# Performance work log

Hardware: AMD Instinct MI355X
Metric: run time of the kernel (lower is better)

The kernel has to match this reference:

```python
import jax, jax.numpy as jnp
import numpy as np

B, S, E, H, STEPS = 32, 2048, 300, 256, 24


def setup_inputs() -> dict:
    key = jax.random.key(0)
    ks = jax.random.split(key, 16)
    sc = 0.05
    inp = {
        "input_ids": jax.random.normal(ks[0], (B, S, E), dtype=jnp.float32),
        "tree_ids": jax.random.randint(ks[1], (B, STEPS, S), 0, S),
        "tree_ids_r": jax.random.randint(ks[2], (B, STEPS, S), 0, S),
        "tree_ids_l": jax.random.randint(ks[3], (B, STEPS, S), 0, S),
        # N-ary (binary) TreeLSTM parameters (Tai et al. 2015)
        "W_iou": jax.random.normal(ks[4], (E, 3 * H), dtype=jnp.float32) * sc,
        "b_iou": jnp.zeros((3 * H,), dtype=jnp.float32),
        "U_iou_l": jax.random.normal(ks[5], (H, 3 * H), dtype=jnp.float32) * sc,
        "U_iou_r": jax.random.normal(ks[6], (H, 3 * H), dtype=jnp.float32) * sc,
        "W_f": jax.random.normal(ks[7], (E, H), dtype=jnp.float32) * sc,
        "b_f": jnp.zeros((H,), dtype=jnp.float32),
        "U_f_ll": jax.random.normal(ks[8], (H, H), dtype=jnp.float32) * sc,
        "U_f_lr": jax.random.normal(ks[9], (H, H), dtype=jnp.float32) * sc,
        "U_f_rl": jax.random.normal(ks[10], (H, H), dtype=jnp.float32) * sc,
        "U_f_rr": jax.random.normal(ks[11], (H, H), dtype=jnp.float32) * sc,
    }
    return inp


def _gather_nodes(t, idx):
    # t: [B,S,H], idx: [B,S] -> [B,S,H]
    return jnp.take_along_axis(t, idx[..., None], axis=1)


def reference(input_ids, tree_ids, tree_ids_r, tree_ids_l,
              W_iou, b_iou, U_iou_l, U_iou_r,
              W_f, b_f, U_f_ll, U_f_lr, U_f_rl, U_f_rr):
    dt = input_ids.dtype
    h0 = jnp.zeros((B, S, H), dtype=dt)
    c0 = jnp.zeros((B, S, H), dtype=dt)
    # input projections are step-invariant: compute once
    x_iou = input_ids @ W_iou + b_iou          # [B,S,3H]
    x_f = input_ids @ W_f + b_f                # [B,S,H]
    bidx = jnp.arange(B)[:, None]              # [B,1]

    def step(carry, ids):
        h, c = carry
        idd, idl, idr = ids                    # each [B,S]
        h_l = _gather_nodes(h, idl); c_l = _gather_nodes(c, idl)
        h_r = _gather_nodes(h, idr); c_r = _gather_nodes(c, idr)
        iou = x_iou + h_l @ U_iou_l + h_r @ U_iou_r
        i, o, u = jnp.split(iou, 3, axis=-1)
        i = jax.nn.sigmoid(i); o = jax.nn.sigmoid(o); u = jnp.tanh(u)
        f_l = jax.nn.sigmoid(x_f + h_l @ U_f_ll + h_r @ U_f_lr)
        f_r = jax.nn.sigmoid(x_f + h_l @ U_f_rl + h_r @ U_f_rr)
        c_new = i * u + f_l * c_l + f_r * c_r
        h_new = o * jnp.tanh(c_new)
        # scatter updates to destination node ids; slot 0 is the null slot
        h = h.at[bidx, idd].set(h_new)
        c = c.at[bidx, idd].set(c_new)
        h = h.at[:, 0].set(0.0)
        c = c.at[:, 0].set(0.0)
        return (h, c), None

    ids_seq = (jnp.transpose(tree_ids, (1, 0, 2)),
               jnp.transpose(tree_ids_l, (1, 0, 2)),
               jnp.transpose(tree_ids_r, (1, 0, 2)))
    (h, c), _ = jax.lax.scan(step, (h0, c0), ids_seq)

    roots = tree_ids[:, -1, :].max(axis=1)     # [B]
    h_root = jnp.take_along_axis(
        h, jnp.broadcast_to(roots[:, None, None], (B, 1, H)), axis=1)[:, 0]
    return (h, c, h_root)
```

## Files before the change

### kernel.cpp

```cpp
#include <hip/hip_runtime.h>
#include <hip/hip_bf16.h>
#include <math.h>

#define B_     32
#define S_     2048
#define E_     300
#define H_     256
#define STEPS_ 24
#define BS_    (B_ * S_)
#define NPACK  1280
#define KSL    16
#define KSLP   10
#define COPYB  1024

typedef __bf16 bf16x8 __attribute__((ext_vector_type(8)));
typedef float  f32x4  __attribute__((ext_vector_type(4)));

__device__ __forceinline__ float sigm(float x) {
    return 1.0f / (1.0f + __expf(-x));
}
__device__ __forceinline__ float fast_tanh(float x) {
    return 2.0f * sigm(2.0f * x) - 1.0f;
}

__global__ __launch_bounds__(256) void pack_B_kernel(
    const float* __restrict__ U_iou_l, const float* __restrict__ U_iou_r,
    const float* __restrict__ U_f_ll,  const float* __restrict__ U_f_lr,
    const float* __restrict__ U_f_rl,  const float* __restrict__ U_f_rr,
    __hip_bfloat16* __restrict__ Bp)
{
    const int idx = blockIdx.x * 256 + threadIdx.x;
    if (idx >= KSL * NPACK * 32) return;
    const int ks = idx / (NPACK * 32);
    const int rem = idx - ks * (NPACK * 32);
    const int p = rem >> 5;
    const int kin = rem & 31;
    const int k = ks * 32 + kin;
    const int w = p / 80;
    const int rg = p - w * 80;
    const int g = rg >> 4;
    const int c = w * 16 + (rg & 15);
    float v;
    if (g < 3) {
        const int col = g * 256 + c;
        v = (k < 256) ? U_iou_l[k * 768 + col] : U_iou_r[(k - 256) * 768 + col];
    } else if (g == 3) {
        v = (k < 256) ? U_f_ll[k * 256 + c] : U_f_lr[(k - 256) * 256 + c];
    } else {
        v = (k < 256) ? U_f_rl[k * 256 + c] : U_f_rr[(k - 256) * 256 + c];
    }
    Bp[idx] = __float2bfloat16(v);
}

__global__ __launch_bounds__(256) void pack_W_kernel(
    const float* __restrict__ W_iou, const float* __restrict__ W_f,
    __hip_bfloat16* __restrict__ Wp)
{
    const int idx = blockIdx.x * 256 + threadIdx.x;
    if (idx >= KSLP * 1024 * 32) return;
    const int ks = idx / (1024 * 32);
    const int rem = idx - ks * (1024 * 32);
    const int p = rem >> 5;
    const int kin = rem & 31;
    const int k = ks * 32 + kin;
    const int cw = p >> 6;
    const int g = (p >> 4) & 3;
    const int col = cw * 16 + (p & 15);
    float v = 0.f;
    if (k < E_) v = (g < 3) ? W_iou[k * 768 + g * 256 + col] : W_f[k * 256 + col];
    Wp[idx] = __float2bfloat16(v);
}

__global__ __launch_bounds__(256) void winner_kernel(
    const int* __restrict__ tree_ids, int* __restrict__ winner)
{
    const int idx = blockIdx.x * 256 + threadIdx.x;
    if (idx >= B_ * STEPS_ * S_) return;
    const int b = idx / (STEPS_ * S_);
    const int rem = idx - b * (STEPS_ * S_);
    const int t = rem / S_;
    const int s = rem - t * S_;
    const int d = tree_ids[idx];
    if ((unsigned)d < (unsigned)S_)
        atomicMax(&winner[(size_t)t * BS_ + b * S_ + d], s);
}

__global__ __launch_bounds__(256) void compact_kernel(
    const int* __restrict__ winner, int* __restrict__ compact,
    int* __restrict__ count)
{
    const int tb = blockIdx.x;
    const int tid = threadIdx.x;
    const int* w = winner + (size_t)tb * S_;
    int* cmp = compact + (size_t)tb * S_;
    __shared__ int scan_[256];
    __shared__ int base_;
    if (tid == 0) base_ = 0;
    __syncthreads();
    for (int chunk = 0; chunk < S_ / 256; ++chunk) {
        const int d = chunk * 256 + tid;
        const int s = w[d];
        const int p = (d != 0 && s >= 0) ? 1 : 0;
        int v = p;
        scan_[tid] = v;
        __syncthreads();
        for (int off = 1; off < 256; off <<= 1) {
            const int add = (tid >= off) ? scan_[tid - off] : 0;
            __syncthreads();
            v += add;
            scan_[tid] = v;
            __syncthreads();
        }
        const int mybase = base_;
        if (p) cmp[mybase + v - 1] = (s << 11) | d;
        __syncthreads();
        if (tid == 0) base_ += scan_[255];
        __syncthreads();
    }
    if (tid == 0) count[tb] = base_;
}

__global__ __launch_bounds__(256) void proj_kernel(
    const float* __restrict__ input, const __hip_bfloat16* __restrict__ Wp,
    const float* __restrict__ b_iou, const float* __restrict__ b_f,
    __hip_bfloat16* __restrict__ x_pack)
{
    __shared__ __hip_bfloat16 Ash[16][328];
    const int tid = threadIdx.x;
    const int row0 = blockIdx.x * 16;

    for (int it = 0; it < 5; ++it) {
        const int idx = tid + it * 256;
        const int r = idx / 80;
        const int c4 = idx - r * 80;
        float4 v = make_float4(0.f, 0.f, 0.f, 0.f);
        if (c4 < 75) v = *(const float4*)(input + (size_t)(row0 + r) * E_ + c4 * 4);
        union { __hip_bfloat16 h[4]; uint2 u; } tconv;
        tconv.h[0] = __float2bfloat16(v.x);
        tconv.h[1] = __float2bfloat16(v.y);
        tconv.h[2] = __float2bfloat16(v.z);
        tconv.h[3] = __float2bfloat16(v.w);
        *(uint2*)&Ash[r][c4 * 4] = tconv.u;
    }
    __syncthreads();

    const int lane = tid & 63;
    const int wave = tid >> 6;
    const int m16 = lane & 15;
    const int q = lane >> 4;

    f32x4 acc[16];
    const f32x4 z4 = {0.f, 0.f, 0.f, 0.f};
#pragma unroll
    for (int nt = 0; nt < 16; ++nt) acc[nt] = z4;

    const __hip_bfloat16* wp = Wp + ((size_t)(wave * 256 + m16)) * 32 + q * 8;
    for (int ks = 0; ks < KSLP; ++ks) {
        const bf16x8 a = *reinterpret_cast<const bf16x8*>(&Ash[m16][ks * 32 + q * 8]);
        const __hip_bfloat16* wk = wp + (size_t)ks * 32768;
#pragma unroll
        for (int nt = 0; nt < 16; ++nt) {
            const bf16x8 bb = *reinterpret_cast<const bf16x8*>(wk + nt * 512);
            acc[nt] = __builtin_amdgcn_mfma_f32_16x16x32_bf16(a, bb, acc[nt], 0, 0, 0);
        }
    }

#pragma unroll
    for (int j = 0; j < 4; ++j) {
        const int row = row0 + q * 4 + j;
        const size_t xrow = (size_t)row * 1024;
#pragma unroll
        for (int chunk = 0; chunk < 4; ++chunk) {
            const int c = (wave * 4 + chunk) * 16 + m16;
            union { __hip_bfloat16 h[4]; uint2 u; } pk;
            pk.h[0] = __float2bfloat16(acc[chunk * 4 + 0][j] + b_iou[c]);
            pk.h[1] = __float2bfloat16(acc[chunk * 4 + 1][j] + b_iou[256 + c]);
            pk.h[2] = __float2bfloat16(acc[chunk * 4 + 2][j] + b_iou[512 + c]);
            pk.h[3] = __float2bfloat16(acc[chunk * 4 + 3][j] + b_f[c]);
            *(uint2*)(x_pack + xrow + (size_t)c * 4) = pk.u;
        }
    }
}

__global__ __launch_bounds__(256, 3) void step_kernel(
    const __hip_bfloat16* __restrict__ h_cur, const __hip_bfloat16* __restrict__ c_cur,
    __hip_bfloat16* __restrict__ h_next, __hip_bfloat16* __restrict__ c_next,
    const int* __restrict__ tree_ids_l, const int* __restrict__ tree_ids_r,
    const int* __restrict__ winner_t, const int* __restrict__ compact,
    const int* __restrict__ count, const __hip_bfloat16* __restrict__ x_pack,
    const __hip_bfloat16* __restrict__ Bp, int t)
{
    const int tid = threadIdx.x;

    if (blockIdx.x < COPYB) {
        const uint4* h_cur4 = (const uint4*)h_cur;
        const uint4* c_cur4 = (const uint4*)c_cur;
        uint4* h_next4 = (uint4*)h_next;
        uint4* c_next4 = (uint4*)c_next;
#pragma unroll
        for (int i = 0; i < 8; ++i) {
            const int idx = blockIdx.x * 256 + tid + i * (COPYB * 256);
            const int row = idx >> 5;
            const int d = row & (S_ - 1);
            if (d == 0) {
                const uint4 z = make_uint4(0u, 0u, 0u, 0u);
                h_next4[idx] = z;
                c_next4[idx] = z;
            } else if (winner_t[row] < 0) {
                h_next4[idx] = h_cur4[idx];
                c_next4[idx] = c_cur4[idx];
            }
        }
        return;
    }

    const int sb     = blockIdx.x - COPYB;
    const int grp    = sb >> 4;
    const int l16    = sb & 15;
    const int nh     = l16 >> 3;
    const int tile_g = grp * 8 + (l16 & 7);
    const int b    = tile_g >> 6;
    const int tile = tile_g & 63;
    const int nAct = count[t * B_ + b];
    const int s0 = tile * 32;
    if (s0 >= nAct) return;

    __shared__ __hip_bfloat16 Ash[32][520];
    __shared__ __hip_bfloat16 Csh[2][32][136];
    __shared__ int sS[32], sD[32], sIdl[32], sIdr[32];

    const int* cmp = compact + ((size_t)(t * B_ + b)) * S_;
    if (tid < 32) {
        const int gi = s0 + tid;
        const int pair = (gi < nAct) ? cmp[gi] : 0;
        sS[tid] = pair >> 11;
        sD[tid] = pair & 2047;
    }
    __syncthreads();

    const int* idl_b = tree_ids_l + ((size_t)b * STEPS_ + t) * S_;
    const int* idr_b = tree_ids_r + ((size_t)b * STEPS_ + t) * S_;
    if (tid < 32)       sIdl[tid]      = idl_b[sS[tid]];
    else if (tid < 64)  sIdr[tid - 32] = idr_b[sS[tid - 32]];
    __syncthreads();

#pragma unroll
    for (int it = 0; it < 12; ++it) {
        const int idx = tid + it * 256;
        if (idx < 2048) {
            const int r = idx >> 6;
            const int ch = idx & 63;
            const int half = ch >> 5;
            const int c16 = ch & 31;
            const int src = half ? sIdr[r] : sIdl[r];
            const uint4 v = *(const uint4*)(h_cur + ((size_t)(b * S_) + src) * H_ + c16 * 8);
            *(uint4*)&Ash[r][half * 256 + c16 * 8] = v;
        } else {
            const int idx2 = idx - 2048;
            const int r = idx2 >> 5;
            const int ch = idx2 & 31;
            const int half = ch >> 4;
            const int c16 = ch & 15;
            const int src = half ? sIdr[r] : sIdl[r];
            const uint4 v = *(const uint4*)(c_cur + ((size_t)(b * S_) + src) * H_
                                            + nh * 128 + c16 * 8);
            *(uint4*)&Csh[half][r][c16 * 8] = v;
        }
    }
    __syncthreads();

    const int lane = tid & 63;
    const int wave = tid >> 6;
    const int m16 = lane & 15;
    const int q = lane >> 4;

    f32x4 acc[2][2][5];
#pragma unroll
    for (int sm = 0; sm < 2; ++sm) {
#pragma unroll
        for (int j = 0; j < 4; ++j) {
            const int r = sm * 16 + q * 4 + j;
            const size_t xrow = ((size_t)(b * S_ + sS[r])) * 1024;
            const bool w = sD[r] != 0;
#pragma unroll
            for (int wg = 0; wg < 2; ++wg) {
                const int cg = nh * 128 + (wave * 2 + wg) * 16 + m16;
                float xi = 0.f, xo = 0.f, xu = 0.f, xf = 0.f;
                if (w) {
                    union { uint2 u; __hip_bfloat16 x[4]; } xv;
                    xv.u = *(const uint2*)(x_pack + xrow + (size_t)cg * 4);
                    xi = __bfloat162float(xv.x[0]);
                    xo = __bfloat162float(xv.x[1]);
                    xu = __bfloat162float(xv.x[2]);
                    xf = __bfloat162float(xv.x[3]);
                }
                acc[sm][wg][0][j] = xi;
                acc[sm][wg][1][j] = xo;
                acc[sm][wg][2][j] = xu;
                acc[sm][wg][3][j] = xf;
                acc[sm][wg][4][j] = xf;
            }
        }
    }

    const __hip_bfloat16* bp_base =
        Bp + ((size_t)((nh * 8 + wave * 2) * 80 + m16)) * 32 + q * 8;

    for (int ks = 0; ks < KSL; ++ks) {
        const bf16x8 a0 = *reinterpret_cast<const bf16x8*>(&Ash[m16][ks * 32 + q * 8]);
        const bf16x8 a1 = *reinterpret_cast<const bf16x8*>(&Ash[16 + m16][ks * 32 + q * 8]);
        const __hip_bfloat16* bk = bp_base + (size_t)ks * (NPACK * 32);
#pragma unroll
        for (int wg = 0; wg < 2; ++wg) {
            bf16x8 bfrag[5];
#pragma unroll
            for (int g = 0; g < 5; ++g)
                bfrag[g] = *reinterpret_cast<const bf16x8*>(bk + (wg * 80 + g * 16) * 32);
#pragma unroll
            for (int g = 0; g < 5; ++g) {
                acc[0][wg][g] = __builtin_amdgcn_mfma_f32_16x16x32_bf16(a0, bfrag[g], acc[0][wg][g], 0, 0, 0);
                acc[1][wg][g] = __builtin_amdgcn_mfma_f32_16x16x32_bf16(a1, bfrag[g], acc[1][wg][g], 0, 0, 0);
            }
        }
    }

#pragma unroll
    for (int sm = 0; sm < 2; ++sm) {
#pragma unroll
        for (int j = 0; j < 4; ++j) {
            const int r = sm * 16 + q * 4 + j;
            const int d = sD[r];
            if (d == 0) continue;
            const size_t orow = ((size_t)(b * S_ + d)) * H_;
#pragma unroll
            for (int wg = 0; wg < 2; ++wg) {
                const int cl_ = (wave * 2 + wg) * 16 + m16;
                const int cg = nh * 128 + cl_;
                const float ig = sigm(acc[sm][wg][0][j]);
                const float og = sigm(acc[sm][wg][1][j]);
                const float ug = fast_tanh(acc[sm][wg][2][j]);
                const float fl = sigm(acc[sm][wg][3][j]);
                const float fr = sigm(acc[sm][wg][4][j]);
                const float cl = __bfloat162float(Csh[0][r][cl_]);
                const float cr = __bfloat162float(Csh[1][r][cl_]);
                const float cn = ig * ug + fl * cl + fr * cr;
                const float hn = og * fast_tanh(cn);
                c_next[orow + cg] = __float2bfloat16(cn);
                h_next[orow + cg] = __float2bfloat16(hn);
            }
        }
    }
}

__global__ __launch_bounds__(256) void convert_kernel(
    const __hip_bfloat16* __restrict__ h, const __hip_bfloat16* __restrict__ c,
    float* __restrict__ out_h, float* __restrict__ out_c)
{
    const size_t i = ((size_t)blockIdx.x * 256 + threadIdx.x) * 8;
#pragma unroll
    for (int j = 0; j < 8; ++j) {
        out_h[i + j] = __bfloat162float(h[i + j]);
        out_c[i + j] = __bfloat162float(c[i + j]);
    }
}

__global__ __launch_bounds__(256) void root_kernel(
    const int* __restrict__ tree_ids,
    const __hip_bfloat16* __restrict__ h, float* __restrict__ h_root)
{
    const int b = blockIdx.x;
    const int tid = threadIdx.x;
    const int* ids = tree_ids + ((size_t)b * STEPS_ + (STEPS_ - 1)) * S_;
    __shared__ int red[256];
    int m = 0;
    for (int s = tid; s < S_; s += 256) m = max(m, ids[s]);
    red[tid] = m;
    __syncthreads();
    for (int off = 128; off > 0; off >>= 1) {
        if (tid < off) red[tid] = max(red[tid], red[tid + off]);
        __syncthreads();
    }
    const int root = red[0];
    h_root[(size_t)b * H_ + tid] =
        __bfloat162float(h[((size_t)(b * S_) + root) * H_ + tid]);
}

extern "C" void kernel_launch(void* const* d_in, const int* in_sizes, int n_in,
                              void* d_out, int out_size, void* d_ws, size_t ws_size,
                              hipStream_t stream)
{
    const float* input_ids  = (const float*)d_in[0];
    const int*   tree_ids   = (const int*)d_in[1];
    const int*   tree_ids_r = (const int*)d_in[2];
    const int*   tree_ids_l = (const int*)d_in[3];
    const float* W_iou   = (const float*)d_in[4];
    const float* b_iou   = (const float*)d_in[5];
    const float* U_iou_l = (const float*)d_in[6];
    const float* U_iou_r = (const float*)d_in[7];
    const float* W_f     = (const float*)d_in[8];
    const float* b_f     = (const float*)d_in[9];
    const float* U_f_ll  = (const float*)d_in[10];
    const float* U_f_lr  = (const float*)d_in[11];
    const float* U_f_rl  = (const float*)d_in[12];
    const float* U_f_rr  = (const float*)d_in[13];

    float* out = (float*)d_out;
    float* out_h = out;
    float* out_c = out + (size_t)BS_ * H_;
    float* out_root = out + (size_t)2 * BS_ * H_;

    char* ws = (char*)d_ws;
    __hip_bfloat16* x_pack = (__hip_bfloat16*)(ws);
    __hip_bfloat16* hA     = (__hip_bfloat16*)(ws + 134217728ull);
    __hip_bfloat16* cA     = (__hip_bfloat16*)(ws + 167772160ull);
    int*            winner = (int*)(ws + 201326592ull);
    __hip_bfloat16* Bp     = (__hip_bfloat16*)(ws + 207618048ull);
    __hip_bfloat16* Wp     = (__hip_bfloat16*)(ws + 208928768ull);
    __hip_bfloat16* hB     = (__hip_bfloat16*)out_h;
    __hip_bfloat16* cB     = (__hip_bfloat16*)out_c;
    int* compact = (int*)((char*)out_h + 33554432ull);
    int* cnt     = compact + (size_t)STEPS_ * B_ * S_;

    hipMemsetAsync(hA, 0, (size_t)BS_ * H_ * sizeof(__hip_bfloat16), stream);
    hipMemsetAsync(cA, 0, (size_t)BS_ * H_ * sizeof(__hip_bfloat16), stream);
    hipMemsetAsync(winner, 0xFF, (size_t)STEPS_ * BS_ * sizeof(int), stream);

    pack_B_kernel<<<(KSL * NPACK * 32 + 255) / 256, 256, 0, stream>>>(
        U_iou_l, U_iou_r, U_f_ll, U_f_lr, U_f_rl, U_f_rr, Bp);
    pack_W_kernel<<<(KSLP * 1024 * 32 + 255) / 256, 256, 0, stream>>>(W_iou, W_f, Wp);
    winner_kernel<<<(B_ * STEPS_ * S_) / 256, 256, 0, stream>>>(tree_ids, winner);
    compact_kernel<<<STEPS_ * B_, 256, 0, stream>>>(winner, compact, cnt);
    proj_kernel<<<BS_ / 16, 256, 0, stream>>>(input_ids, Wp, b_iou, b_f, x_pack);

    for (int t = 0; t < STEPS_; ++t) {
        const __hip_bfloat16* hc = (t & 1) ? hB : hA;
        const __hip_bfloat16* cc = (t & 1) ? cB : cA;
        __hip_bfloat16*       hn = (t & 1) ? hA : hB;
        __hip_bfloat16*       cn = (t & 1) ? cA : cB;
        const int* wt = winner + (size_t)t * BS_;

        step_kernel<<<COPYB + B_ * 64 * 2, 256, 0, stream>>>(
            hc, cc, hn, cn, tree_ids_l, tree_ids_r, wt,
            compact, cnt, x_pack, Bp, t);
    }

    convert_kernel<<<(BS_ * H_ / 8) / 256, 256, 0, stream>>>(hA, cA, out_h, out_c);
    root_kernel<<<B_, 256, 0, stream>>>(tree_ids, hA, out_root);
}
```

Baseline: 5.062 ms.

## Split step kernel into four column quarters per tile and load c directly

Each 32-row tile is now split across four blocks, each covering 64 hidden columns, instead of two blocks of 128 columns. Each wave therefore handles one 16-column group, which halves the accumulators and raises the occupancy hint from 3 to 4. The shared-memory staging of c_l/c_r is dropped in favour of direct global reads in the epilogue. The cost is that every block still gathers the full 32x512 h operand, so h gather traffic and A-fragment LDS reads double per tile.

```diff
diff --git a/kernel.cpp b/kernel.cpp
--- a/kernel.cpp
+++ b/kernel.cpp
@@ -182,7 +182,7 @@
     }
 }
 
-__global__ __launch_bounds__(256, 3) void step_kernel(
+__global__ __launch_bounds__(256, 4) void step_kernel(
     const __hip_bfloat16* __restrict__ h_cur, const __hip_bfloat16* __restrict__ c_cur,
     __hip_bfloat16* __restrict__ h_next, __hip_bfloat16* __restrict__ c_next,
     const int* __restrict__ tree_ids_l, const int* __restrict__ tree_ids_r,
@@ -215,10 +215,10 @@
     }
 
     const int sb     = blockIdx.x - COPYB;
-    const int grp    = sb >> 4;
-    const int l16    = sb & 15;
-    const int nh     = l16 >> 3;
-    const int tile_g = grp * 8 + (l16 & 7);
+    const int grp    = sb >> 5;
+    const int l32    = sb & 31;
+    const int nq     = l32 >> 3;
+    const int tile_g = grp * 8 + (l32 & 7);
     const int b    = tile_g >> 6;
     const int tile = tile_g & 63;
     const int nAct = count[t * B_ + b];
@@ -226,7 +226,6 @@
     if (s0 >= nAct) return;
 
     __shared__ __hip_bfloat16 Ash[32][520];
-    __shared__ __hip_bfloat16 Csh[2][32][136];
     __shared__ int sS[32], sD[32], sIdl[32], sIdr[32];
 
     const int* cmp = compact + ((size_t)(t * B_ + b)) * S_;
@@ -245,27 +244,15 @@
     __syncthreads();
 
 #pragma unroll
-    for (int it = 0; it < 12; ++it) {
+    for (int it = 0; it < 8; ++it) {
         const int idx = tid + it * 256;
-        if (idx < 2048) {
-            const int r = idx >> 6;
-            const int ch = idx & 63;
-            const int half = ch >> 5;
-            const int c16 = ch & 31;
-            const int src = half ? sIdr[r] : sIdl[r];
-            const uint4 v = *(const uint4*)(h_cur + ((size_t)(b * S_) + src) * H_ + c16 * 8);
-            *(uint4*)&Ash[r][half * 256 + c16 * 8] = v;
-        } else {
-            const int idx2 = idx - 2048;
-            const int r = idx2 >> 5;
-            const int ch = idx2 & 31;
-            const int half = ch >> 4;
-            const int c16 = ch & 15;
-            const int src = half ? sIdr[r] : sIdl[r];
-            const uint4 v = *(const uint4*)(c_cur + ((size_t)(b * S_) + src) * H_
-                                            + nh * 128 + c16 * 8);
-            *(uint4*)&Csh[half][r][c16 * 8] = v;
-        }
+        const int r = idx >> 6;
+        const int ch = idx & 63;
+        const int half = ch >> 5;
+        const int c16 = ch & 31;
+        const int src = half ? sIdr[r] : sIdl[r];
+        const uint4 v = *(const uint4*)(h_cur + ((size_t)(b * S_) + src) * H_ + c16 * 8);
+        *(uint4*)&Ash[r][half * 256 + c16 * 8] = v;
     }
     __syncthreads();
 
@@ -273,57 +260,52 @@
     const int wave = tid >> 6;
     const int m16 = lane & 15;
     const int q = lane >> 4;
-
-    f32x4 acc[2][2][5];
+    const int w16 = nq * 4 + wave;
+    const int cg = w16 * 16 + m16;
+
+    f32x4 acc[2][5];
 #pragma unroll
     for (int sm = 0; sm < 2; ++sm) {
 #pragma unroll
         for (int j = 0; j < 4; ++j) {
             const int r = sm * 16 + q * 4 + j;
-            const size_t xrow = ((size_t)(b * S_ + sS[r])) * 1024;
-            const bool w = sD[r] != 0;
-#pragma unroll
-            for (int wg = 0; wg < 2; ++wg) {
-                const int cg = nh * 128 + (wave * 2 + wg) * 16 + m16;
-                float xi = 0.f, xo = 0.f, xu = 0.f, xf = 0.f;
-                if (w) {
-                    union { uint2 u; __hip_bfloat16 x[4]; } xv;
-                    xv.u = *(const uint2*)(x_pack + xrow + (size_t)cg * 4);
-                    xi = __bfloat162float(xv.x[0]);
-                    xo = __bfloat162float(xv.x[1]);
-                    xu = __bfloat162float(xv.x[2]);
-                    xf = __bfloat162float(xv.x[3]);
-                }
-                acc[sm][wg][0][j] = xi;
-                acc[sm][wg][1][j] = xo;
-                acc[sm][wg][2][j] = xu;
-                acc[sm][wg][3][j] = xf;
-                acc[sm][wg][4][j] = xf;
+            float xi = 0.f, xo = 0.f, xu = 0.f, xf = 0.f;
+            if (sD[r] != 0) {
+                const size_t xrow = ((size_t)(b * S_ + sS[r])) * 1024;
+                union { uint2 u; __hip_bfloat16 x[4]; } xv;
+                xv.u = *(const uint2*)(x_pack + xrow + (size_t)cg * 4);
+                xi = __bfloat162float(xv.x[0]);
+                xo = __bfloat162float(xv.x[1]);
+                xu = __bfloat162float(xv.x[2]);
+                xf = __bfloat162float(xv.x[3]);
             }
+            acc[sm][0][j] = xi;
+            acc[sm][1][j] = xo;
+            acc[sm][2][j] = xu;
+            acc[sm][3][j] = xf;
+            acc[sm][4][j] = xf;
         }
     }
 
     const __hip_bfloat16* bp_base =
-        Bp + ((size_t)((nh * 8 + wave * 2) * 80 + m16)) * 32 + q * 8;
+        Bp + ((size_t)(w16 * 80 + m16)) * 32 + q * 8;
 
     for (int ks = 0; ks < KSL; ++ks) {
         const bf16x8 a0 = *reinterpret_cast<const bf16x8*>(&Ash[m16][ks * 32 + q * 8]);
         const bf16x8 a1 = *reinterpret_cast<const bf16x8*>(&Ash[16 + m16][ks * 32 + q * 8]);
         const __hip_bfloat16* bk = bp_base + (size_t)ks * (NPACK * 32);
-#pragma unroll
-        for (int wg = 0; wg < 2; ++wg) {
-            bf16x8 bfrag[5];
-#pragma unroll
-            for (int g = 0; g < 5; ++g)
-                bfrag[g] = *reinterpret_cast<const bf16x8*>(bk + (wg * 80 + g * 16) * 32);
-#pragma unroll
-            for (int g = 0; g < 5; ++g) {
-                acc[0][wg][g] = __builtin_amdgcn_mfma_f32_16x16x32_bf16(a0, bfrag[g], acc[0][wg][g], 0, 0, 0);
-                acc[1][wg][g] = __builtin_amdgcn_mfma_f32_16x16x32_bf16(a1, bfrag[g], acc[1][wg][g], 0, 0, 0);
-            }
-        }
-    }
-
+        bf16x8 bfrag[5];
+#pragma unroll
+        for (int g = 0; g < 5; ++g)
+            bfrag[g] = *reinterpret_cast<const bf16x8*>(bk + g * 512);
+#pragma unroll
+        for (int g = 0; g < 5; ++g) {
+            acc[0][g] = __builtin_amdgcn_mfma_f32_16x16x32_bf16(a0, bfrag[g], acc[0][g], 0, 0, 0);
+            acc[1][g] = __builtin_amdgcn_mfma_f32_16x16x32_bf16(a1, bfrag[g], acc[1][g], 0, 0, 0);
+        }
+    }
+
+    const __hip_bfloat16* cb = c_cur + (size_t)(b * S_) * H_ + cg;
 #pragma unroll
     for (int sm = 0; sm < 2; ++sm) {
 #pragma unroll
@@ -332,22 +314,17 @@
             const int d = sD[r];
             if (d == 0) continue;
             const size_t orow = ((size_t)(b * S_ + d)) * H_;
-#pragma unroll
-            for (int wg = 0; wg < 2; ++wg) {
-                const int cl_ = (wave * 2 + wg) * 16 + m16;
-                const int cg = nh * 128 + cl_;
-                const float ig = sigm(acc[sm][wg][0][j]);
-                const float og = sigm(acc[sm][wg][1][j]);
-                const float ug = fast_tanh(acc[sm][wg][2][j]);
-                const float fl = sigm(acc[sm][wg][3][j]);
-                const float fr = sigm(acc[sm][wg][4][j]);
-                const float cl = __bfloat162float(Csh[0][r][cl_]);
-                const float cr = __bfloat162float(Csh[1][r][cl_]);
-                const float cn = ig * ug + fl * cl + fr * cr;
-                const float hn = og * fast_tanh(cn);
-                c_next[orow + cg] = __float2bfloat16(cn);
-                h_next[orow + cg] = __float2bfloat16(hn);
-            }
+            const float ig = sigm(acc[sm][0][j]);
+            const float og = sigm(acc[sm][1][j]);
+            const float ug = fast_tanh(acc[sm][2][j]);
+            const float fl = sigm(acc[sm][3][j]);
+            const float fr = sigm(acc[sm][4][j]);
+            const float cl = __bfloat162float(cb[(size_t)sIdl[r] * H_]);
+            const float cr = __bfloat162float(cb[(size_t)sIdr[r] * H_]);
+            const float cn = ig * ug + fl * cl + fr * cr;
+            const float hn = og * fast_tanh(cn);
+            c_next[orow + cg] = __float2bfloat16(cn);
+            h_next[orow + cg] = __float2bfloat16(hn);
         }
     }
 }
@@ -439,7 +416,7 @@
         __hip_bfloat16*       cn = (t & 1) ? cA : cB;
         const int* wt = winner + (size_t)t * BS_;
 
-        step_kernel<<<COPYB + B_ * 64 * 2, 256, 0, stream>>>(
+        step_kernel<<<COPYB + B_ * 64 * 4, 256, 0, stream>>>(
             hc, cc, hn, cn, tree_ids_l, tree_ids_r, wt,
             compact, cnt, x_pack, Bp, t);
     }
```

Measured after the change: 4.763 ms. 5.9% less time.
